# Optimization experiments

Hardware: AMD Instinct MI355X
Metric: run time of the kernel (lower is better)

## Reference

```python
import jax, jax.numpy as jnp
import numpy as np

KS = 3          # kernel_size
PAD = KS // 2   # =1, symmetric pad (pd=2, pdr=1 in the original)


def setup_inputs() -> dict:
    key = jax.random.key(0)
    k1, k2 = jax.random.split(key)
    B, H, W, T, C = 1, 48, 48, 48, 32
    q = jax.random.normal(k1, (B, H, W, T, C), dtype=jnp.float32)
    k = jax.random.normal(k2, (B, H, W, T, C), dtype=jnp.float32)
    return {"q": q, "k": k}


def reference(q, k):
    # q, k: [B, H, W, T, C]
    B, H, W, T, C = q.shape
    # zero-pad k spatially by 1 on each side (matches nnf.pad with pdr=1)
    kp = jnp.pad(k, ((0, 0), (PAD, PAD), (PAD, PAD), (PAD, PAD), (0, 0)))
    # gather the 27 shifted windows; token order (dh major, dt minor) matches
    # unfold(1).unfold(2).unfold(3) + permute in the original.
    wins = jnp.stack(
        [kp[:, a:a + H, b:b + W, c:c + T, :]
         for a in range(KS) for b in range(KS) for c in range(KS)],
        axis=4,
    )  # [B, H, W, T, 27, C]
    # QK^T over channel dim -> [B, H, W, T, 27]
    scores = jnp.einsum('bhwtc,bhwtjc->bhwtj', q, wins)
    attn = jax.nn.softmax(scores, axis=-1)
    # fixed displacement grid v: offsets (-1,0,1)^3 in (dh, dw, dt) order
    ax = jnp.arange(-(KS // 2), KS // 2 + 1, dtype=q.dtype)  # [-1, 0, 1]
    offs = jnp.stack(jnp.meshgrid(ax, ax, ax, indexing='ij'), axis=-1)
    offs = offs.reshape(KS ** 3, 3)  # [27, 3]
    # displacement-weighted sum -> [B, H, W, T, 3]
    x = jnp.einsum('bhwtj,jd->bhwtd', attn, offs)
    # -> [B, 3, H, W, T]
    return jnp.transpose(x, (0, 4, 1, 2, 3))
```

## Files before the change

### kernel.cpp

```cpp
#include <hip/hip_runtime.h>
#include <hip/hip_bf16.h>
#include <math.h>

#define DH 48
#define DW 48
#define DT 48
#define DC 32
#define NPOS (DH * DW * DT)

#define TH 4
#define TW 4
#define TT 4
#define LH (TH + 2)
#define LW (TW + 2)
#define LT (TT + 2)
#define NLINES (LH * LW * LT)
#define NF4 (NLINES * 8)
#define NTHREADS 256

typedef __attribute__((address_space(3))) unsigned int lds_u32_t;
typedef const __attribute__((address_space(1))) unsigned int glb_u32_t;

template <int CTRL>
__device__ __forceinline__ float qperm_add(float v) {
    const int s = __builtin_amdgcn_update_dpp(
        0, __float_as_int(v), CTRL, 0xF, 0xF, true);
    return v + __int_as_float(s);
}

__global__ __launch_bounds__(NTHREADS, 5) void cotr_natt_kernel(
    const float* __restrict__ q,
    const float* __restrict__ k,
    float* __restrict__ out)
{
    __shared__ __align__(16) float kl[NF4 * 4];

    const int bt = blockIdx.x % (DT / TT);
    const int bw = (blockIdx.x / (DT / TT)) % (DW / TW);
    const int bh = blockIdx.x / ((DT / TT) * (DW / TW));
    const int h0 = bh * TH, w0 = bw * TW, t0 = bt * TT;

    const int tid = threadIdx.x;

#pragma unroll
    for (int i = 0; i < 7; ++i) {
        const int s = i * NTHREADS + tid;
        if (s < NF4) {
            const int line = s >> 3, c4 = s & 7;
            const int llt = line % LT;
            const int lhw = line / LT;
            const int llw = lhw % LW;
            const int llh = lhw / LW;
            const int hh = min(max(h0 + llh - 1, 0), DH - 1);
            const int ww = min(max(w0 + llw - 1, 0), DW - 1);
            const int tt = min(max(t0 + llt - 1, 0), DT - 1);
            const float* gp =
                k + ((size_t)(hh * DW + ww) * DT + tt) * DC + c4 * 4;
            __builtin_amdgcn_global_load_lds((glb_u32_t*)gp,
                                             (lds_u32_t*)&kl[s * 4], 16, 0, 0);
        }
    }

    const int p = tid >> 2;
    const int sub = tid & 3;
    const int lt = p & 3;
    const int lw = (p >> 2) & 3;
    const int lh = p >> 4;
    const int h = h0 + lh, w = w0 + lw, t = t0 + lt;
    const int idx = (h * DW + w) * DT + t;

    const float4* qp = reinterpret_cast<const float4*>(q + (size_t)idx * DC);
    const float4 qa = qp[sub * 2];
    const float4 qb = qp[sub * 2 + 1];

    float as_[3], bs_[3], cs_[3];
#pragma unroll
    for (int u = 0; u < 3; ++u) {
        as_[u] = ((unsigned)(h + u - 1) < DH) ? 1.0f : 0.0f;
        bs_[u] = ((unsigned)(w + u - 1) < DW) ? 1.0f : 0.0f;
        cs_[u] = ((unsigned)(t + u - 1) < DT) ? 1.0f : 0.0f;
    }

    __syncthreads();

    float sum = 0.f, oh = 0.f, ow = 0.f, ot = 0.f;
#pragma unroll
    for (int a = 0; a < 3; ++a) {
#pragma unroll
        for (int b = 0; b < 3; ++b) {
            const float sab = as_[a] * bs_[b];
#pragma unroll
            for (int c = 0; c < 3; ++c) {
                const int line = ((lh + a) * LW + (lw + b)) * LT + (lt + c);
                const float4* kp =
                    reinterpret_cast<const float4*>(&kl[line * DC]);
                const float4 ka = kp[sub * 2];
                const float4 kb = kp[sub * 2 + 1];
                float d =
                    fmaf(qa.x, ka.x,
                    fmaf(qa.y, ka.y,
                    fmaf(qa.z, ka.z,
                    fmaf(qa.w, ka.w,
                    fmaf(qb.x, kb.x,
                    fmaf(qb.y, kb.y,
                    fmaf(qb.z, kb.z, qb.w * kb.w)))))));
                d = qperm_add<0xB1>(d);
                d = qperm_add<0x4E>(d);
                const float e = __expf(d * (sab * cs_[c]));
                sum += e;
                if (a == 0) oh -= e;
                if (a == 2) oh += e;
                if (b == 0) ow -= e;
                if (b == 2) ow += e;
                if (c == 0) ot -= e;
                if (c == 2) ot += e;
            }
        }
    }

    const float inv = 1.0f / sum;

    if (sub == 0)      out[0 * NPOS + idx] = oh * inv;
    else if (sub == 1) out[1 * NPOS + idx] = ow * inv;
    else if (sub == 2) out[2 * NPOS + idx] = ot * inv;
}

extern "C" void kernel_launch(void* const* d_in, const int* in_sizes, int n_in,
                              void* d_out, int out_size, void* d_ws, size_t ws_size,
                              hipStream_t stream) {
    const float* q = reinterpret_cast<const float*>(d_in[0]);
    const float* k = reinterpret_cast<const float*>(d_in[1]);
    float* out = reinterpret_cast<float*>(d_out);

    const int blocks = (DH / TH) * (DW / TW) * (DT / TT);
    cotr_natt_kernel<<<blocks, NTHREADS, 0, stream>>>(q, k, out);
}
```

Measured before the change: 78.33 us.

## Process two adjacent T positions per thread group sharing K LDS reads

Doubles the tile along T to 8 and has each 4-thread group compute two neighbouring output positions. Each group walks a 4-line window along T instead of 3 per position, so each K line read from LDS serves both positions (12 loads instead of 18). The halo overhead per tile also shrinks. In exchange, blocks are halved, LDS per block grows, occupancy drops, and register pressure rises from the extra q values and accumulators.

```diff
diff --git a/kernel.cpp b/kernel.cpp
--- a/kernel.cpp
+++ b/kernel.cpp
@@ -10,7 +10,7 @@
 
 #define TH 4
 #define TW 4
-#define TT 4
+#define TT 8
 #define LH (TH + 2)
 #define LW (TW + 2)
 #define LT (TT + 2)
@@ -28,12 +28,12 @@
     return v + __int_as_float(s);
 }
 
-__global__ __launch_bounds__(NTHREADS, 5) void cotr_natt_kernel(
+__global__ __launch_bounds__(NTHREADS, 3) void cotr_natt_kernel(
     const float* __restrict__ q,
     const float* __restrict__ k,
     float* __restrict__ out)
 {
-    __shared__ __align__(16) float kl[NF4 * 4];
+    __shared__ __align__(16) float kl[NLINES * DC];
 
     const int bt = blockIdx.x % (DT / TT);
     const int bw = (blockIdx.x / (DT / TT)) % (DW / TW);
@@ -43,7 +43,7 @@
     const int tid = threadIdx.x;
 
 #pragma unroll
-    for (int i = 0; i < 7; ++i) {
+    for (int i = 0; i < 12; ++i) {
         const int s = i * NTHREADS + tid;
         if (s < NF4) {
             const int line = s >> 3, c4 = s & 7;
@@ -61,68 +61,97 @@
         }
     }
 
-    const int p = tid >> 2;
     const int sub = tid & 3;
-    const int lt = p & 3;
-    const int lw = (p >> 2) & 3;
-    const int lh = p >> 4;
-    const int h = h0 + lh, w = w0 + lw, t = t0 + lt;
-    const int idx = (h * DW + w) * DT + t;
+    const int pair = tid >> 2;
+    const int ltp = pair & 3;
+    const int lw = (pair >> 2) & 3;
+    const int lh = pair >> 4;
+    const int lt0 = ltp * 2;
+    const int h = h0 + lh, w = w0 + lw, tb = t0 + lt0;
+    const int idx0 = (h * DW + w) * DT + tb;
 
-    const float4* qp = reinterpret_cast<const float4*>(q + (size_t)idx * DC);
-    const float4 qa = qp[sub * 2];
-    const float4 qb = qp[sub * 2 + 1];
+    const float4* qp = reinterpret_cast<const float4*>(q + (size_t)idx0 * DC);
+    const float4 qA0 = qp[sub * 2],     qA1 = qp[sub * 2 + 1];
+    const float4 qB0 = qp[8 + sub * 2], qB1 = qp[8 + sub * 2 + 1];
 
-    float as_[3], bs_[3], cs_[3];
+    float as_[3], bs_[3], tv[4];
 #pragma unroll
     for (int u = 0; u < 3; ++u) {
         as_[u] = ((unsigned)(h + u - 1) < DH) ? 1.0f : 0.0f;
         bs_[u] = ((unsigned)(w + u - 1) < DW) ? 1.0f : 0.0f;
-        cs_[u] = ((unsigned)(t + u - 1) < DT) ? 1.0f : 0.0f;
     }
+#pragma unroll
+    for (int l = 0; l < 4; ++l)
+        tv[l] = ((unsigned)(tb - 1 + l) < DT) ? 1.0f : 0.0f;
 
     __syncthreads();
 
-    float sum = 0.f, oh = 0.f, ow = 0.f, ot = 0.f;
+    float s0 = 0.f, oh0 = 0.f, ow0 = 0.f, ot0 = 0.f;
+    float s1 = 0.f, oh1 = 0.f, ow1 = 0.f, ot1 = 0.f;
 #pragma unroll
     for (int a = 0; a < 3; ++a) {
 #pragma unroll
         for (int b = 0; b < 3; ++b) {
             const float sab = as_[a] * bs_[b];
+            const int lbase = ((lh + a) * LW + (lw + b)) * LT + lt0;
 #pragma unroll
-            for (int c = 0; c < 3; ++c) {
-                const int line = ((lh + a) * LW + (lw + b)) * LT + (lt + c);
+            for (int l = 0; l < 4; ++l) {
                 const float4* kp =
-                    reinterpret_cast<const float4*>(&kl[line * DC]);
+                    reinterpret_cast<const float4*>(&kl[(lbase + l) * DC]);
                 const float4 ka = kp[sub * 2];
                 const float4 kb = kp[sub * 2 + 1];
-                float d =
-                    fmaf(qa.x, ka.x,
-                    fmaf(qa.y, ka.y,
-                    fmaf(qa.z, ka.z,
-                    fmaf(qa.w, ka.w,
-                    fmaf(qb.x, kb.x,
-                    fmaf(qb.y, kb.y,
-                    fmaf(qb.z, kb.z, qb.w * kb.w)))))));
-                d = qperm_add<0xB1>(d);
-                d = qperm_add<0x4E>(d);
-                const float e = __expf(d * (sab * cs_[c]));
-                sum += e;
-                if (a == 0) oh -= e;
-                if (a == 2) oh += e;
-                if (b == 0) ow -= e;
-                if (b == 2) ow += e;
-                if (c == 0) ot -= e;
-                if (c == 2) ot += e;
+                const float sc = sab * tv[l];
+                if (l <= 2) {
+                    float d =
+                        fmaf(qA0.x, ka.x, fmaf(qA0.y, ka.y,
+                        fmaf(qA0.z, ka.z, fmaf(qA0.w, ka.w,
+                        fmaf(qA1.x, kb.x, fmaf(qA1.y, kb.y,
+                        fmaf(qA1.z, kb.z, qA1.w * kb.w)))))));
+                    d = qperm_add<0xB1>(d);
+                    d = qperm_add<0x4E>(d);
+                    const float e = __expf(d * sc);
+                    s0 += e;
+                    if (a == 0) oh0 -= e;
+                    if (a == 2) oh0 += e;
+                    if (b == 0) ow0 -= e;
+                    if (b == 2) ow0 += e;
+                    if (l == 0) ot0 -= e;
+                    if (l == 2) ot0 += e;
+                }
+                if (l >= 1) {
+                    float d =
+                        fmaf(qB0.x, ka.x, fmaf(qB0.y, ka.y,
+                        fmaf(qB0.z, ka.z, fmaf(qB0.w, ka.w,
+                        fmaf(qB1.x, kb.x, fmaf(qB1.y, kb.y,
+                        fmaf(qB1.z, kb.z, qB1.w * kb.w)))))));
+                    d = qperm_add<0xB1>(d);
+                    d = qperm_add<0x4E>(d);
+                    const float e = __expf(d * sc);
+                    s1 += e;
+                    if (a == 0) oh1 -= e;
+                    if (a == 2) oh1 += e;
+                    if (b == 0) ow1 -= e;
+                    if (b == 2) ow1 += e;
+                    if (l == 1) ot1 -= e;
+                    if (l == 3) ot1 += e;
+                }
             }
         }
     }
 
-    const float inv = 1.0f / sum;
+    const float i0 = 1.0f / s0;
+    const float i1 = 1.0f / s1;
 
-    if (sub == 0)      out[0 * NPOS + idx] = oh * inv;
-    else if (sub == 1) out[1 * NPOS + idx] = ow * inv;
-    else if (sub == 2) out[2 * NPOS + idx] = ot * inv;
+    if (sub == 0) {
+        out[0 * NPOS + idx0]     = oh0 * i0;
+        out[0 * NPOS + idx0 + 1] = oh1 * i1;
+    } else if (sub == 1) {
+        out[1 * NPOS + idx0]     = ow0 * i0;
+        out[1 * NPOS + idx0 + 1] = ow1 * i1;
+    } else if (sub == 2) {
+        out[2 * NPOS + idx0]     = ot0 * i0;
+        out[2 * NPOS + idx0 + 1] = ot1 * i1;
+    }
 }
 
 extern "C" void kernel_launch(void* const* d_in, const int* in_sizes, int n_in,
```

Measured after the change: 80.21 us. 2.4% more time.
